# Optimization experiments

Hardware: AMD Instinct MI355X
Metric: run time of the kernel (lower is better)

Reference implementation:

```python
import jax, jax.numpy as jnp
import numpy as np

HID_GNN = 64
HID_LSTM = 128
FUTURE = 24
N_HYDRO = 32
N_METEO = 64
B, T, E = 32, 168, 384
SLOPE = 0.01  # F.leaky_relu default


def setup_inputs() -> dict:
    key = jax.random.key(0)
    ks = jax.random.split(key, 12)
    N = N_HYDRO + N_METEO
    data_meteo = jax.random.normal(ks[0], (B, T, N_METEO, 1), jnp.float32)
    data_hydro = jax.random.normal(ks[1], (B, T, N_HYDRO, 1), jnp.float32)
    edge_index = jax.random.randint(ks[2], (2, E), 0, N, dtype=jnp.int64)
    # GraphConv(1, HID_GNN): out = lin_root(x) + lin_rel(sum_j x_j) + bias
    W_root = jax.random.normal(ks[3], (HID_GNN, 1), jnp.float32) * 1.0
    W_rel = jax.random.normal(ks[4], (HID_GNN, 1), jnp.float32) * 1.0
    b_gnn = jnp.zeros((HID_GNN,), jnp.float32)
    # Per-station LSTM weights (torch gate order i,f,g,o), stacked over stations
    sih = 1.0 / np.sqrt(HID_GNN)
    shh = 1.0 / np.sqrt(HID_LSTM)
    Wih = jax.random.normal(ks[5], (N_HYDRO, 4 * HID_LSTM, HID_GNN), jnp.float32) * sih
    Whh = jax.random.normal(ks[6], (N_HYDRO, 4 * HID_LSTM, HID_LSTM), jnp.float32) * shh
    bih = jnp.zeros((N_HYDRO, 4 * HID_LSTM), jnp.float32)
    bhh = jnp.zeros((N_HYDRO, 4 * HID_LSTM), jnp.float32)
    W_lin = jax.random.normal(ks[7], (FUTURE, HID_LSTM), jnp.float32) * shh
    b_lin = jnp.zeros((FUTURE,), jnp.float32)
    return {"data_meteo": data_meteo, "data_hydro": data_hydro, "edge_index": edge_index,
            "W_root": W_root, "W_rel": W_rel, "b_gnn": b_gnn,
            "Wih": Wih, "Whh": Whh, "bih": bih, "bhh": bhh,
            "W_lin": W_lin, "b_lin": b_lin}


def _lstm_last(xs, Wih_s, Whh_s, b_s):
    # xs: [B,T,D]; one station's LSTM; returns last hidden [B,H]
    H = Whh_s.shape[1]
    h0 = jnp.zeros((xs.shape[0], H), xs.dtype)

    def step(carry, xt):
        h, c = carry
        gates = xt @ Wih_s.T + h @ Whh_s.T + b_s  # [B,4H]
        i, f, g, o = jnp.split(gates, 4, axis=-1)
        c = jax.nn.sigmoid(f) * c + jax.nn.sigmoid(i) * jnp.tanh(g)
        h = jax.nn.sigmoid(o) * jnp.tanh(c)
        return (h, c), None

    (hT, _), _ = jax.lax.scan(step, (h0, h0), jnp.swapaxes(xs, 0, 1))
    return hT


def reference(data_meteo, data_hydro, edge_index, W_root, W_rel, b_gnn,
              Wih, Whh, bih, bhh, W_lin, b_lin):
    Bn, Tn, Nh, F = data_hydro.shape
    Nm = data_meteo.shape[2]
    N = Nh + Nm
    # [B,T,N,1] -> one graph per (b,t); same edge_index in every graph
    x = jnp.concatenate([data_hydro, data_meteo], axis=2).reshape(Bn * Tn, N, F)
    src, dst = edge_index[0], edge_index[1]
    agg = jnp.zeros_like(x).at[:, dst].add(x[:, src])  # sum aggregation
    h = x @ W_root.T + agg @ W_rel.T + b_gnn          # GraphConv, [G,N,HID_GNN]
    h = jax.nn.leaky_relu(h, SLOPE)
    hydro = h.reshape(Bn, Tn, N, -1)[:, :, :Nh, :]    # [B,T,Nh,HID_GNN]
    # per-station LSTM: vmap over station axis with station-specific weights
    last = jax.vmap(_lstm_last, in_axes=(2, 0, 0, 0))(hydro, Wih, Whh, bih + bhh)  # [Nh,B,H]
    pred = last @ W_lin.T + b_lin                     # [Nh,B,FUTURE]
    pred = jnp.swapaxes(pred, 0, 1)                   # [B,Nh,FUTURE]
    return jax.nn.leaky_relu(pred, SLOPE)
```

## Files before the change

### kernel.cpp

```cpp
#include <hip/hip_runtime.h>

typedef unsigned short u16;
typedef unsigned int u32;
typedef __attribute__((ext_vector_type(8))) short short8;
typedef __attribute__((ext_vector_type(4))) float floatx4;
typedef __attribute__((ext_vector_type(4))) float float4v;

#define B_ 32
#define T_ 168
#define NH_ 32
#define NM_ 64
#define E_ 384
#define HL_ 128
#define FUT_ 24
#define SLOPE_ 0.01f
#define XP_ 80
#define HP_ 144
#define WIH_LP 72
#define WHH_LP 136
#define OVL_E (T_ * 4 * XP_)

static __device__ __forceinline__ float b2f(u16 u) {
  u32 v = ((u32)u) << 16;
  return __builtin_bit_cast(float, v);
}
static __device__ __forceinline__ u16 f2bf(float f) {
  u32 x = __builtin_bit_cast(u32, f);
  u32 r = (x + 0x7fffu + ((x >> 16) & 1u)) >> 16;
  return (u16)r;
}
static __device__ __forceinline__ float fexp2(float x) { return __builtin_amdgcn_exp2f(x); }
static __device__ __forceinline__ float frcp(float x) { return __builtin_amdgcn_rcpf(x); }
static __device__ __forceinline__ float sigm(float x) {
  return frcp(1.0f + fexp2(-1.4426950408889634f * x));
}
static __device__ __forceinline__ float tanh_fast(float x) {
  return 1.0f - 2.0f * frcp(1.0f + fexp2(2.8853900817779268f * x));
}
static __device__ __forceinline__ float sel4(floatx4 v, int r) {
  float m0 = (r & 1) ? v[1] : v[0];
  float m1 = (r & 1) ? v[3] : v[2];
  return (r & 2) ? m1 : m0;
}
static __device__ __forceinline__ float lrelu(float x) { return fmaxf(x, SLOPE_ * x); }

__launch_bounds__(512, 2)
__global__ void fused_kernel(const float* __restrict__ dm, const float* __restrict__ dh,
                             const int* __restrict__ eidx,
                             const float* __restrict__ Wroot, const float* __restrict__ Wrel,
                             const float* __restrict__ bgnn,
                             const float* __restrict__ Wih, const float* __restrict__ Whh,
                             const float* __restrict__ bih, const float* __restrict__ bhh,
                             const float* __restrict__ Wlin, const float* __restrict__ blin,
                             float* __restrict__ out) {
  const int s = blockIdx.x & 31;
  const int bg = blockIdx.x >> 5;
  const int tid = threadIdx.x;
  const int w = tid >> 6;
  const int lane = tid & 63;
  const int cm = lane & 15;
  const int q = lane >> 4;
  const int b = cm & 3;
  const int rho = cm >> 2;

  __shared__ __align__(16) u16 ovl[OVL_E];
  __shared__ __align__(16) u16 hbuf[2 * 4 * HP_];
  __shared__ float xh_lds[4][T_];
  __shared__ float ag_lds[4][T_];
  __shared__ float wr_s[64], wv_s[64], bg_s[64];
  __shared__ int srcs[E_];
  __shared__ int nsrc, iflag;

  if (tid == 0) { nsrc = 0; iflag = 0; }
  for (int i = tid; i < 2 * 4 * HP_; i += 512) hbuf[i] = 0;
  __syncthreads();

  {
    int odd = 0;
    for (int e = tid; e < E_; e += 512) odd |= eidx[2 * e + 1];
    if (odd) atomicOr(&iflag, 1);
  }
  __syncthreads();
  const bool i32 = iflag != 0;

  for (int e = tid; e < E_; e += 512) {
    int se = i32 ? eidx[e] : eidx[2 * e];
    int de = i32 ? eidx[E_ + e] : eidx[2 * E_ + 2 * e];
    if (de == s) { int i = atomicAdd(&nsrc, 1); srcs[i] = se; }
  }
  if (tid < 64) { wr_s[tid] = Wroot[tid]; wv_s[tid] = Wrel[tid]; bg_s[tid] = bgnn[tid]; }
  for (int i = tid; i < 4 * T_; i += 512) {
    int bb = i / T_, t = i % T_;
    xh_lds[bb][t] = dh[((size_t)(bg * 4 + bb) * T_ + t) * NH_ + s];
  }
  floatx4 bias_init[4];
#pragma unroll
  for (int blk = 0; blk < 4; blk++)
#pragma unroll
    for (int r = 0; r < 4; r++) {
      const int nb = blk * 128 + w * 16 + q * 4 + r;
      bias_init[blk][r] = bih[s * 512 + nb] + bhh[s * 512 + nb];
    }
  __syncthreads();

  const int ns = nsrc;
  for (int i = tid; i < 4 * T_; i += 512) {
    int bb = i / T_, t = i % T_;
    size_t gb = (size_t)(bg * 4 + bb) * T_ + t;
    float a = 0.f;
    for (int j = 0; j < ns; j++) {
      int sr = srcs[j];
      a += (sr < NH_) ? dh[gb * NH_ + sr] : dm[gb * NM_ + (sr - NH_)];
    }
    ag_lds[bb][t] = a;
  }

  short8 Af[4][6];
  const int nl = w * 16 + cm;
  __syncthreads();
  {
    const float* g = Wih + (size_t)s * 512 * 64;
#pragma unroll
    for (int it = 0; it < 16; it++) {
      int j = tid + it * 512;
      float4v v = *(const float4v*)(g + 4 * j);
      u16* dst = ovl + (j >> 4) * WIH_LP + (j & 15) * 4;
      dst[0] = f2bf(v[0]); dst[1] = f2bf(v[1]); dst[2] = f2bf(v[2]); dst[3] = f2bf(v[3]);
    }
  }
  __syncthreads();
#pragma unroll
  for (int blk = 0; blk < 4; blk++)
#pragma unroll
    for (int kk = 0; kk < 2; kk++)
      Af[blk][kk] = *(const short8*)(ovl + (blk * 128 + nl) * WIH_LP + kk * 32 + q * 8);
  __syncthreads();
  {
    const float* g = Whh + (size_t)s * 512 * 128;
#pragma unroll
    for (int it = 0; it < 16; it++) {
      int j = tid + it * 512;
      float4v v = *(const float4v*)(g + 4 * j);
      u16* dst = ovl + (j >> 5) * WHH_LP + (j & 31) * 4;
      dst[0] = f2bf(v[0]); dst[1] = f2bf(v[1]); dst[2] = f2bf(v[2]); dst[3] = f2bf(v[3]);
    }
  }
  __syncthreads();
#pragma unroll
  for (int blk = 0; blk < 2; blk++)
#pragma unroll
    for (int kk = 0; kk < 4; kk++)
      Af[blk][2 + kk] = *(const short8*)(ovl + (blk * 128 + nl) * WHH_LP + kk * 32 + q * 8);
  __syncthreads();
  {
    const float* g = Whh + ((size_t)s * 512 + 256) * 128;
#pragma unroll
    for (int it = 0; it < 16; it++) {
      int j = tid + it * 512;
      float4v v = *(const float4v*)(g + 4 * j);
      u16* dst = ovl + (j >> 5) * WHH_LP + (j & 31) * 4;
      dst[0] = f2bf(v[0]); dst[1] = f2bf(v[1]); dst[2] = f2bf(v[2]); dst[3] = f2bf(v[3]);
    }
  }
  __syncthreads();
#pragma unroll
  for (int blk = 2; blk < 4; blk++)
#pragma unroll
    for (int kk = 0; kk < 4; kk++)
      Af[blk][2 + kk] = *(const short8*)(ovl + ((blk - 2) * 128 + nl) * WHH_LP + kk * 32 + q * 8);
  __syncthreads();

  {
    const int k = tid & 63;
    const int bb = (tid >> 6) & 3;
    const int th = tid >> 8;
    const float wrk = wr_s[k], wvk = wv_s[k], bgk = bg_s[k];
    for (int i = 0; i < T_ / 2; i++) {
      const int t = th * (T_ / 2) + i;
      const float xv = xh_lds[bb][t] * wrk + ag_lds[bb][t] * wvk + bgk;
      ovl[t * (4 * XP_) + bb * XP_ + k] = f2bf(lrelu(xv));
    }
  }
  __syncthreads();

  floatx4 accN[4];
  {
    short8 Bx0 = *(const short8*)(ovl + b * XP_ + q * 8);
    short8 Bx1 = *(const short8*)(ovl + b * XP_ + 32 + q * 8);
#pragma unroll
    for (int blk = 0; blk < 4; blk++) {
      accN[blk] = __builtin_amdgcn_mfma_f32_16x16x32_bf16(Af[blk][0], Bx0, bias_init[blk], 0, 0, 0);
      accN[blk] = __builtin_amdgcn_mfma_f32_16x16x32_bf16(Af[blk][1], Bx1, accN[blk], 0, 0, 0);
    }
  }
  float c = 0.0f;
#pragma unroll 2
  for (int t = 0; t < T_; t++) {
    const int p = t & 1, pn = p ^ 1;
    short8 Bh[4];
#pragma unroll
    for (int kk = 0; kk < 4; kk++)
      Bh[kk] = *(const short8*)(hbuf + p * (4 * HP_) + b * HP_ + kk * 32 + q * 8);

    floatx4 acc[4];
#pragma unroll
    for (int blk = 0; blk < 4; blk++) acc[blk] = accN[blk];
#pragma unroll
    for (int kk = 0; kk < 4; kk++)
#pragma unroll
      for (int blk = 0; blk < 4; blk++)
        acc[blk] = __builtin_amdgcn_mfma_f32_16x16x32_bf16(Af[blk][2 + kk], Bh[kk], acc[blk], 0, 0, 0);

    const float gi = sel4(acc[0], rho);
    const float gf = sel4(acc[1], rho);
    const float gg = sel4(acc[2], rho);
    const float go = sel4(acc[3], rho);
    c = sigm(gf) * c + sigm(gi) * tanh_fast(gg);
    const float hh = sigm(go) * tanh_fast(c);
    hbuf[pn * (4 * HP_) + b * HP_ + w * 16 + q * 4 + rho] = f2bf(hh);

    if (t + 1 < T_) {
      short8 Bx0 = *(const short8*)(ovl + (t + 1) * (4 * XP_) + b * XP_ + q * 8);
      short8 Bx1 = *(const short8*)(ovl + (t + 1) * (4 * XP_) + b * XP_ + 32 + q * 8);
#pragma unroll
      for (int blk = 0; blk < 4; blk++) {
        accN[blk] = __builtin_amdgcn_mfma_f32_16x16x32_bf16(Af[blk][0], Bx0, bias_init[blk], 0, 0, 0);
        accN[blk] = __builtin_amdgcn_mfma_f32_16x16x32_bf16(Af[blk][1], Bx1, accN[blk], 0, 0, 0);
      }
    }
    __syncthreads();
  }

  if (tid < 4 * FUT_) {
    const int bb = tid / FUT_;
    const int f = tid % FUT_;
    float a = blin[f];
#pragma unroll 8
    for (int k = 0; k < HL_; k++) a += b2f(hbuf[bb * HP_ + k]) * Wlin[f * HL_ + k];
    out[((size_t)(bg * 4 + bb) * NH_ + s) * FUT_ + f] = lrelu(a);
  }
}

extern "C" void kernel_launch(void* const* d_in, const int* in_sizes, int n_in,
                              void* d_out, int out_size, void* d_ws, size_t ws_size,
                              hipStream_t stream) {
  const float* dm = (const float*)d_in[0];
  const float* dh = (const float*)d_in[1];
  const int* eidx = (const int*)d_in[2];
  const float* Wroot = (const float*)d_in[3];
  const float* Wrel = (const float*)d_in[4];
  const float* bgnn = (const float*)d_in[5];
  const float* Wih = (const float*)d_in[6];
  const float* Whh = (const float*)d_in[7];
  const float* bih = (const float*)d_in[8];
  const float* bhh = (const float*)d_in[9];
  const float* Wlin = (const float*)d_in[10];
  const float* blin = (const float*)d_in[11];
  float* out = (float*)d_out;

  fused_kernel<<<256, 512, 0, stream>>>(dm, dh, eidx, Wroot, Wrel, bgnn, Wih, Whh,
                                        bih, bhh, Wlin, blin, out);
}
```

Baseline: 190.7 us.

## Interleave two independent batch streams per block and prescale gate weights

Each block now handles 8 batch rows as two independent 4-row LSTM streams. The MFMA work of one stream is interleaved with the gate math of the other, which hides the serial recurrence latency, and the grid shrinks from 256 to 128 blocks. The input projection is computed over two 84-step windows so the shared-memory buffer fits. Sigmoid and tanh scale factors are folded into the bf16 weights and biases to remove one multiply per gate. The cost is half as many blocks, so fewer CUs are in use, plus higher register pressure.

```diff
diff --git a/kernel.cpp b/kernel.cpp
--- a/kernel.cpp
+++ b/kernel.cpp
@@ -16,9 +16,11 @@
 #define SLOPE_ 0.01f
 #define XP_ 80
 #define HP_ 144
+#define TW_ 84
 #define WIH_LP 72
 #define WHH_LP 136
-#define OVL_E (T_ * 4 * XP_)
+#define CH1_ (-1.4426950408889634f)
+#define CH2_ (2.8853900817779268f)
 
 static __device__ __forceinline__ float b2f(u16 u) {
   u32 v = ((u32)u) << 16;
@@ -31,9 +33,8 @@
 }
 static __device__ __forceinline__ float fexp2(float x) { return __builtin_amdgcn_exp2f(x); }
 static __device__ __forceinline__ float frcp(float x) { return __builtin_amdgcn_rcpf(x); }
-static __device__ __forceinline__ float sigm(float x) {
-  return frcp(1.0f + fexp2(-1.4426950408889634f * x));
-}
+static __device__ __forceinline__ float sigm_pre(float x) { return frcp(1.0f + fexp2(x)); }
+static __device__ __forceinline__ float tanh_pre(float x) { return 1.0f - 2.0f * frcp(1.0f + fexp2(x)); }
 static __device__ __forceinline__ float tanh_fast(float x) {
   return 1.0f - 2.0f * frcp(1.0f + fexp2(2.8853900817779268f * x));
 }
@@ -54,7 +55,7 @@
                              const float* __restrict__ Wlin, const float* __restrict__ blin,
                              float* __restrict__ out) {
   const int s = blockIdx.x & 31;
-  const int bg = blockIdx.x >> 5;
+  const int bgp = blockIdx.x >> 5;
   const int tid = threadIdx.x;
   const int w = tid >> 6;
   const int lane = tid & 63;
@@ -63,16 +64,16 @@
   const int b = cm & 3;
   const int rho = cm >> 2;
 
-  __shared__ __align__(16) u16 ovl[OVL_E];
-  __shared__ __align__(16) u16 hbuf[2 * 4 * HP_];
-  __shared__ float xh_lds[4][T_];
-  __shared__ float ag_lds[4][T_];
+  __shared__ __align__(16) u16 xwin[TW_ * 8 * XP_];
+  __shared__ __align__(16) u16 hbuf[2 * 2 * 4 * HP_];
+  __shared__ float xh_lds[8][T_];
+  __shared__ float ag_lds[8][T_];
   __shared__ float wr_s[64], wv_s[64], bg_s[64];
   __shared__ int srcs[E_];
   __shared__ int nsrc, iflag;
 
   if (tid == 0) { nsrc = 0; iflag = 0; }
-  for (int i = tid; i < 2 * 4 * HP_; i += 512) hbuf[i] = 0;
+  for (int i = tid; i < 2 * 2 * 4 * HP_; i += 512) hbuf[i] = 0;
   __syncthreads();
 
   {
@@ -89,24 +90,26 @@
     if (de == s) { int i = atomicAdd(&nsrc, 1); srcs[i] = se; }
   }
   if (tid < 64) { wr_s[tid] = Wroot[tid]; wv_s[tid] = Wrel[tid]; bg_s[tid] = bgnn[tid]; }
-  for (int i = tid; i < 4 * T_; i += 512) {
+  for (int i = tid; i < 8 * T_; i += 512) {
     int bb = i / T_, t = i % T_;
-    xh_lds[bb][t] = dh[((size_t)(bg * 4 + bb) * T_ + t) * NH_ + s];
+    xh_lds[bb][t] = dh[((size_t)(bgp * 8 + bb) * T_ + t) * NH_ + s];
   }
   floatx4 bias_init[4];
 #pragma unroll
-  for (int blk = 0; blk < 4; blk++)
+  for (int blk = 0; blk < 4; blk++) {
+    const float sc = (blk == 2) ? CH2_ : CH1_;
 #pragma unroll
     for (int r = 0; r < 4; r++) {
       const int nb = blk * 128 + w * 16 + q * 4 + r;
-      bias_init[blk][r] = bih[s * 512 + nb] + bhh[s * 512 + nb];
-    }
+      bias_init[blk][r] = (bih[s * 512 + nb] + bhh[s * 512 + nb]) * sc;
+    }
+  }
   __syncthreads();
 
   const int ns = nsrc;
-  for (int i = tid; i < 4 * T_; i += 512) {
+  for (int i = tid; i < 8 * T_; i += 512) {
     int bb = i / T_, t = i % T_;
-    size_t gb = (size_t)(bg * 4 + bb) * T_ + t;
+    size_t gb = (size_t)(bgp * 8 + bb) * T_ + t;
     float a = 0.f;
     for (int j = 0; j < ns; j++) {
       int sr = srcs[j];
@@ -124,8 +127,10 @@
     for (int it = 0; it < 16; it++) {
       int j = tid + it * 512;
       float4v v = *(const float4v*)(g + 4 * j);
-      u16* dst = ovl + (j >> 4) * WIH_LP + (j & 15) * 4;
-      dst[0] = f2bf(v[0]); dst[1] = f2bf(v[1]); dst[2] = f2bf(v[2]); dst[3] = f2bf(v[3]);
+      const float sc = (((j >> 4) >> 7) == 2) ? CH2_ : CH1_;
+      u16* dst = xwin + (j >> 4) * WIH_LP + (j & 15) * 4;
+      dst[0] = f2bf(v[0] * sc); dst[1] = f2bf(v[1] * sc);
+      dst[2] = f2bf(v[2] * sc); dst[3] = f2bf(v[3] * sc);
     }
   }
   __syncthreads();
@@ -133,7 +138,7 @@
   for (int blk = 0; blk < 4; blk++)
 #pragma unroll
     for (int kk = 0; kk < 2; kk++)
-      Af[blk][kk] = *(const short8*)(ovl + (blk * 128 + nl) * WIH_LP + kk * 32 + q * 8);
+      Af[blk][kk] = *(const short8*)(xwin + (blk * 128 + nl) * WIH_LP + kk * 32 + q * 8);
   __syncthreads();
   {
     const float* g = Whh + (size_t)s * 512 * 128;
@@ -141,8 +146,9 @@
     for (int it = 0; it < 16; it++) {
       int j = tid + it * 512;
       float4v v = *(const float4v*)(g + 4 * j);
-      u16* dst = ovl + (j >> 5) * WHH_LP + (j & 31) * 4;
-      dst[0] = f2bf(v[0]); dst[1] = f2bf(v[1]); dst[2] = f2bf(v[2]); dst[3] = f2bf(v[3]);
+      u16* dst = xwin + (j >> 5) * WHH_LP + (j & 31) * 4;
+      dst[0] = f2bf(v[0] * CH1_); dst[1] = f2bf(v[1] * CH1_);
+      dst[2] = f2bf(v[2] * CH1_); dst[3] = f2bf(v[3] * CH1_);
     }
   }
   __syncthreads();
@@ -150,7 +156,7 @@
   for (int blk = 0; blk < 2; blk++)
 #pragma unroll
     for (int kk = 0; kk < 4; kk++)
-      Af[blk][2 + kk] = *(const short8*)(ovl + (blk * 128 + nl) * WHH_LP + kk * 32 + q * 8);
+      Af[blk][2 + kk] = *(const short8*)(xwin + (blk * 128 + nl) * WHH_LP + kk * 32 + q * 8);
   __syncthreads();
   {
     const float* g = Whh + ((size_t)s * 512 + 256) * 128;
@@ -158,8 +164,10 @@
     for (int it = 0; it < 16; it++) {
       int j = tid + it * 512;
       float4v v = *(const float4v*)(g + 4 * j);
-      u16* dst = ovl + (j >> 5) * WHH_LP + (j & 31) * 4;
-      dst[0] = f2bf(v[0]); dst[1] = f2bf(v[1]); dst[2] = f2bf(v[2]); dst[3] = f2bf(v[3]);
+      const float sc = ((j >> 5) < 128) ? CH2_ : CH1_;
+      u16* dst = xwin + (j >> 5) * WHH_LP + (j & 31) * 4;
+      dst[0] = f2bf(v[0] * sc); dst[1] = f2bf(v[1] * sc);
+      dst[2] = f2bf(v[2] * sc); dst[3] = f2bf(v[3] * sc);
     }
   }
   __syncthreads();
@@ -167,77 +175,111 @@
   for (int blk = 2; blk < 4; blk++)
 #pragma unroll
     for (int kk = 0; kk < 4; kk++)
-      Af[blk][2 + kk] = *(const short8*)(ovl + ((blk - 2) * 128 + nl) * WHH_LP + kk * 32 + q * 8);
-  __syncthreads();
-
-  {
-    const int k = tid & 63;
-    const int bb = (tid >> 6) & 3;
-    const int th = tid >> 8;
-    const float wrk = wr_s[k], wvk = wv_s[k], bgk = bg_s[k];
-    for (int i = 0; i < T_ / 2; i++) {
-      const int t = th * (T_ / 2) + i;
-      const float xv = xh_lds[bb][t] * wrk + ag_lds[bb][t] * wvk + bgk;
-      ovl[t * (4 * XP_) + bb * XP_ + k] = f2bf(lrelu(xv));
-    }
-  }
-  __syncthreads();
-
-  floatx4 accN[4];
-  {
-    short8 Bx0 = *(const short8*)(ovl + b * XP_ + q * 8);
-    short8 Bx1 = *(const short8*)(ovl + b * XP_ + 32 + q * 8);
-#pragma unroll
-    for (int blk = 0; blk < 4; blk++) {
-      accN[blk] = __builtin_amdgcn_mfma_f32_16x16x32_bf16(Af[blk][0], Bx0, bias_init[blk], 0, 0, 0);
-      accN[blk] = __builtin_amdgcn_mfma_f32_16x16x32_bf16(Af[blk][1], Bx1, accN[blk], 0, 0, 0);
-    }
-  }
-  float c = 0.0f;
+      Af[blk][2 + kk] = *(const short8*)(xwin + ((blk - 2) * 128 + nl) * WHH_LP + kk * 32 + q * 8);
+
+  float cA = 0.f, cB = 0.f;
+  floatx4 accNA[4];
+#pragma unroll 1
+  for (int ch = 0; ch < 2; ch++) {
+    const int t0 = ch * TW_;
+    __syncthreads();
+    {
+      const int k = tid & 63;
+      const int bb = tid >> 6;
+      const float wrk = wr_s[k], wvk = wv_s[k], bgk = bg_s[k];
+      u16* xw = xwin + bb * XP_ + k;
+#pragma unroll 4
+      for (int i = 0; i < TW_; i++) {
+        const float xv = xh_lds[bb][t0 + i] * wrk + ag_lds[bb][t0 + i] * wvk + bgk;
+        xw[i * (8 * XP_)] = f2bf(lrelu(xv));
+      }
+    }
+    __syncthreads();
+    short8 BxB0, BxB1;
+    {
+      short8 BxA0 = *(const short8*)(xwin + b * XP_ + q * 8);
+      short8 BxA1 = *(const short8*)(xwin + b * XP_ + 32 + q * 8);
+#pragma unroll
+      for (int blk = 0; blk < 4; blk++) {
+        accNA[blk] = __builtin_amdgcn_mfma_f32_16x16x32_bf16(Af[blk][0], BxA0, bias_init[blk], 0, 0, 0);
+        accNA[blk] = __builtin_amdgcn_mfma_f32_16x16x32_bf16(Af[blk][1], BxA1, accNA[blk], 0, 0, 0);
+      }
+      BxB0 = *(const short8*)(xwin + (b + 4) * XP_ + q * 8);
+      BxB1 = *(const short8*)(xwin + (b + 4) * XP_ + 32 + q * 8);
+    }
 #pragma unroll 2
-  for (int t = 0; t < T_; t++) {
-    const int p = t & 1, pn = p ^ 1;
-    short8 Bh[4];
-#pragma unroll
-    for (int kk = 0; kk < 4; kk++)
-      Bh[kk] = *(const short8*)(hbuf + p * (4 * HP_) + b * HP_ + kk * 32 + q * 8);
-
-    floatx4 acc[4];
-#pragma unroll
-    for (int blk = 0; blk < 4; blk++) acc[blk] = accN[blk];
-#pragma unroll
-    for (int kk = 0; kk < 4; kk++)
+    for (int i = 0; i < TW_; i++) {
+      const int p = i & 1, pn = p ^ 1;
+      short8 BhA[4];
+#pragma unroll
+      for (int kk = 0; kk < 4; kk++)
+        BhA[kk] = *(const short8*)(hbuf + (p * 4 + b) * HP_ + kk * 32 + q * 8);
+      floatx4 aB[4];
+#pragma unroll
+      for (int blk = 0; blk < 4; blk++) {
+        aB[blk] = __builtin_amdgcn_mfma_f32_16x16x32_bf16(Af[blk][0], BxB0, bias_init[blk], 0, 0, 0);
+        aB[blk] = __builtin_amdgcn_mfma_f32_16x16x32_bf16(Af[blk][1], BxB1, aB[blk], 0, 0, 0);
+      }
+      floatx4 aA[4];
 #pragma unroll
       for (int blk = 0; blk < 4; blk++)
-        acc[blk] = __builtin_amdgcn_mfma_f32_16x16x32_bf16(Af[blk][2 + kk], Bh[kk], acc[blk], 0, 0, 0);
-
-    const float gi = sel4(acc[0], rho);
-    const float gf = sel4(acc[1], rho);
-    const float gg = sel4(acc[2], rho);
-    const float go = sel4(acc[3], rho);
-    c = sigm(gf) * c + sigm(gi) * tanh_fast(gg);
-    const float hh = sigm(go) * tanh_fast(c);
-    hbuf[pn * (4 * HP_) + b * HP_ + w * 16 + q * 4 + rho] = f2bf(hh);
-
-    if (t + 1 < T_) {
-      short8 Bx0 = *(const short8*)(ovl + (t + 1) * (4 * XP_) + b * XP_ + q * 8);
-      short8 Bx1 = *(const short8*)(ovl + (t + 1) * (4 * XP_) + b * XP_ + 32 + q * 8);
-#pragma unroll
-      for (int blk = 0; blk < 4; blk++) {
-        accN[blk] = __builtin_amdgcn_mfma_f32_16x16x32_bf16(Af[blk][0], Bx0, bias_init[blk], 0, 0, 0);
-        accN[blk] = __builtin_amdgcn_mfma_f32_16x16x32_bf16(Af[blk][1], Bx1, accN[blk], 0, 0, 0);
-      }
-    }
-    __syncthreads();
-  }
-
-  if (tid < 4 * FUT_) {
+        aA[blk] = __builtin_amdgcn_mfma_f32_16x16x32_bf16(Af[blk][2], BhA[0], accNA[blk], 0, 0, 0);
+#pragma unroll
+      for (int kk = 1; kk < 4; kk++)
+#pragma unroll
+        for (int blk = 0; blk < 4; blk++)
+          aA[blk] = __builtin_amdgcn_mfma_f32_16x16x32_bf16(Af[blk][2 + kk], BhA[kk], aA[blk], 0, 0, 0);
+      short8 BhB[4];
+#pragma unroll
+      for (int kk = 0; kk < 4; kk++)
+        BhB[kk] = *(const short8*)(hbuf + ((2 + p) * 4 + b) * HP_ + kk * 32 + q * 8);
+      {
+        const float gi = sel4(aA[0], rho);
+        const float gf = sel4(aA[1], rho);
+        const float gg = sel4(aA[2], rho);
+        const float go = sel4(aA[3], rho);
+        cA = sigm_pre(gf) * cA + sigm_pre(gi) * tanh_pre(gg);
+        const float hh = sigm_pre(go) * tanh_fast(cA);
+        hbuf[(pn * 4 + b) * HP_ + w * 16 + q * 4 + rho] = f2bf(hh);
+      }
+#pragma unroll
+      for (int kk = 0; kk < 4; kk++)
+#pragma unroll
+        for (int blk = 0; blk < 4; blk++)
+          aB[blk] = __builtin_amdgcn_mfma_f32_16x16x32_bf16(Af[blk][2 + kk], BhB[kk], aB[blk], 0, 0, 0);
+      if (i + 1 < TW_) {
+        short8 BxA0 = *(const short8*)(xwin + (i + 1) * (8 * XP_) + b * XP_ + q * 8);
+        short8 BxA1 = *(const short8*)(xwin + (i + 1) * (8 * XP_) + b * XP_ + 32 + q * 8);
+#pragma unroll
+        for (int blk = 0; blk < 4; blk++) {
+          accNA[blk] = __builtin_amdgcn_mfma_f32_16x16x32_bf16(Af[blk][0], BxA0, bias_init[blk], 0, 0, 0);
+          accNA[blk] = __builtin_amdgcn_mfma_f32_16x16x32_bf16(Af[blk][1], BxA1, accNA[blk], 0, 0, 0);
+        }
+        BxB0 = *(const short8*)(xwin + (i + 1) * (8 * XP_) + (b + 4) * XP_ + q * 8);
+        BxB1 = *(const short8*)(xwin + (i + 1) * (8 * XP_) + (b + 4) * XP_ + 32 + q * 8);
+      }
+      {
+        const float gi = sel4(aB[0], rho);
+        const float gf = sel4(aB[1], rho);
+        const float gg = sel4(aB[2], rho);
+        const float go = sel4(aB[3], rho);
+        cB = sigm_pre(gf) * cB + sigm_pre(gi) * tanh_pre(gg);
+        const float hh = sigm_pre(go) * tanh_fast(cB);
+        hbuf[((2 + pn) * 4 + b) * HP_ + w * 16 + q * 4 + rho] = f2bf(hh);
+      }
+      __syncthreads();
+    }
+  }
+
+  if (tid < 8 * FUT_) {
     const int bb = tid / FUT_;
     const int f = tid % FUT_;
+    const int st = bb >> 2, bl = bb & 3;
     float a = blin[f];
 #pragma unroll 8
-    for (int k = 0; k < HL_; k++) a += b2f(hbuf[bb * HP_ + k]) * Wlin[f * HL_ + k];
-    out[((size_t)(bg * 4 + bb) * NH_ + s) * FUT_ + f] = lrelu(a);
+    for (int k = 0; k < HL_; k++)
+      a += b2f(hbuf[(st * 2 * 4 + bl) * HP_ + k]) * Wlin[f * HL_ + k];
+    out[((size_t)(bgp * 8 + bb) * NH_ + s) * FUT_ + f] = lrelu(a);
   }
 }
 
@@ -258,6 +300,6 @@
   const float* blin = (const float*)d_in[11];
   float* out = (float*)d_out;
 
-  fused_kernel<<<256, 512, 0, stream>>>(dm, dh, eidx, Wroot, Wrel, bgnn, Wih, Whh,
+  fused_kernel<<<128, 512, 0, stream>>>(dm, dh, eidx, Wroot, Wrel, bgnn, Wih, Whh,
                                         bih, bhh, Wlin, blin, out);
 }
```

Measured after the change: 270.6 us. +41.9%, slower.

## Split batch into two interleaved MFMA streams and fold activation scales into weights

Applied to the files above, without the earlier changes.

Splits the four batch columns of the recurrent MFMA into two independent two-column streams whose MFMAs are interleaved, giving the per-step dependency chain more independent work to hide MFMA latency. The next step's input projection is issued before the gate nonlinearities. The exp2 scale constants for sigmoid/tanh are pre-multiplied into the bf16 weights and biases, removing multiplies from the per-step activation math. The cost is twice as many MFMA instructions per step, each doing half-useful columns, plus slightly different bf16 rounding of scaled weights.

```diff
diff --git a/kernel.cpp b/kernel.cpp
--- a/kernel.cpp
+++ b/kernel.cpp
@@ -18,7 +18,8 @@
 #define HP_ 144
 #define WIH_LP 72
 #define WHH_LP 136
-#define OVL_E (T_ * 4 * XP_)
+#define CH1_ (-1.4426950408889634f)
+#define CH2_ (2.8853900817779268f)
 
 static __device__ __forceinline__ float b2f(u16 u) {
   u32 v = ((u32)u) << 16;
@@ -31,9 +32,8 @@
 }
 static __device__ __forceinline__ float fexp2(float x) { return __builtin_amdgcn_exp2f(x); }
 static __device__ __forceinline__ float frcp(float x) { return __builtin_amdgcn_rcpf(x); }
-static __device__ __forceinline__ float sigm(float x) {
-  return frcp(1.0f + fexp2(-1.4426950408889634f * x));
-}
+static __device__ __forceinline__ float sigm_pre(float x) { return frcp(1.0f + fexp2(x)); }
+static __device__ __forceinline__ float tanh_pre(float x) { return 1.0f - 2.0f * frcp(1.0f + fexp2(x)); }
 static __device__ __forceinline__ float tanh_fast(float x) {
   return 1.0f - 2.0f * frcp(1.0f + fexp2(2.8853900817779268f * x));
 }
@@ -60,11 +60,12 @@
   const int lane = tid & 63;
   const int cm = lane & 15;
   const int q = lane >> 4;
-  const int b = cm & 3;
-  const int rho = cm >> 2;
-
-  __shared__ __align__(16) u16 ovl[OVL_E];
-  __shared__ __align__(16) u16 hbuf[2 * 4 * HP_];
+  const int b = cm & 1;
+  const int rho = (cm >> 1) & 3;
+  const int str = cm >> 3;
+
+  __shared__ __align__(16) u16 xbuf[T_ * 4 * XP_];
+  __shared__ __align__(16) u16 hbuf[2 * 2 * 2 * HP_];
   __shared__ float xh_lds[4][T_];
   __shared__ float ag_lds[4][T_];
   __shared__ float wr_s[64], wv_s[64], bg_s[64];
@@ -72,7 +73,7 @@
   __shared__ int nsrc, iflag;
 
   if (tid == 0) { nsrc = 0; iflag = 0; }
-  for (int i = tid; i < 2 * 4 * HP_; i += 512) hbuf[i] = 0;
+  for (int i = tid; i < 2 * 2 * 2 * HP_; i += 512) hbuf[i] = 0;
   __syncthreads();
 
   {
@@ -95,12 +96,14 @@
   }
   floatx4 bias_init[4];
 #pragma unroll
-  for (int blk = 0; blk < 4; blk++)
+  for (int blk = 0; blk < 4; blk++) {
+    const float sc = (blk == 2) ? CH2_ : CH1_;
 #pragma unroll
     for (int r = 0; r < 4; r++) {
       const int nb = blk * 128 + w * 16 + q * 4 + r;
-      bias_init[blk][r] = bih[s * 512 + nb] + bhh[s * 512 + nb];
-    }
+      bias_init[blk][r] = (bih[s * 512 + nb] + bhh[s * 512 + nb]) * sc;
+    }
+  }
   __syncthreads();
 
   const int ns = nsrc;
@@ -124,8 +127,10 @@
     for (int it = 0; it < 16; it++) {
       int j = tid + it * 512;
       float4v v = *(const float4v*)(g + 4 * j);
-      u16* dst = ovl + (j >> 4) * WIH_LP + (j & 15) * 4;
-      dst[0] = f2bf(v[0]); dst[1] = f2bf(v[1]); dst[2] = f2bf(v[2]); dst[3] = f2bf(v[3]);
+      const float sc = (((j >> 4) >> 7) == 2) ? CH2_ : CH1_;
+      u16* dst = xbuf + (j >> 4) * WIH_LP + (j & 15) * 4;
+      dst[0] = f2bf(v[0] * sc); dst[1] = f2bf(v[1] * sc);
+      dst[2] = f2bf(v[2] * sc); dst[3] = f2bf(v[3] * sc);
     }
   }
   __syncthreads();
@@ -133,7 +138,7 @@
   for (int blk = 0; blk < 4; blk++)
 #pragma unroll
     for (int kk = 0; kk < 2; kk++)
-      Af[blk][kk] = *(const short8*)(ovl + (blk * 128 + nl) * WIH_LP + kk * 32 + q * 8);
+      Af[blk][kk] = *(const short8*)(xbuf + (blk * 128 + nl) * WIH_LP + kk * 32 + q * 8);
   __syncthreads();
   {
     const float* g = Whh + (size_t)s * 512 * 128;
@@ -141,8 +146,9 @@
     for (int it = 0; it < 16; it++) {
       int j = tid + it * 512;
       float4v v = *(const float4v*)(g + 4 * j);
-      u16* dst = ovl + (j >> 5) * WHH_LP + (j & 31) * 4;
-      dst[0] = f2bf(v[0]); dst[1] = f2bf(v[1]); dst[2] = f2bf(v[2]); dst[3] = f2bf(v[3]);
+      u16* dst = xbuf + (j >> 5) * WHH_LP + (j & 31) * 4;
+      dst[0] = f2bf(v[0] * CH1_); dst[1] = f2bf(v[1] * CH1_);
+      dst[2] = f2bf(v[2] * CH1_); dst[3] = f2bf(v[3] * CH1_);
     }
   }
   __syncthreads();
@@ -150,7 +156,7 @@
   for (int blk = 0; blk < 2; blk++)
 #pragma unroll
     for (int kk = 0; kk < 4; kk++)
-      Af[blk][2 + kk] = *(const short8*)(ovl + (blk * 128 + nl) * WHH_LP + kk * 32 + q * 8);
+      Af[blk][2 + kk] = *(const short8*)(xbuf + (blk * 128 + nl) * WHH_LP + kk * 32 + q * 8);
   __syncthreads();
   {
     const float* g = Whh + ((size_t)s * 512 + 256) * 128;
@@ -158,8 +164,10 @@
     for (int it = 0; it < 16; it++) {
       int j = tid + it * 512;
       float4v v = *(const float4v*)(g + 4 * j);
-      u16* dst = ovl + (j >> 5) * WHH_LP + (j & 31) * 4;
-      dst[0] = f2bf(v[0]); dst[1] = f2bf(v[1]); dst[2] = f2bf(v[2]); dst[3] = f2bf(v[3]);
+      const float sc = ((j >> 5) < 128) ? CH2_ : CH1_;
+      u16* dst = xbuf + (j >> 5) * WHH_LP + (j & 31) * 4;
+      dst[0] = f2bf(v[0] * sc); dst[1] = f2bf(v[1] * sc);
+      dst[2] = f2bf(v[2] * sc); dst[3] = f2bf(v[3] * sc);
     }
   }
   __syncthreads();
@@ -167,7 +175,7 @@
   for (int blk = 2; blk < 4; blk++)
 #pragma unroll
     for (int kk = 0; kk < 4; kk++)
-      Af[blk][2 + kk] = *(const short8*)(ovl + ((blk - 2) * 128 + nl) * WHH_LP + kk * 32 + q * 8);
+      Af[blk][2 + kk] = *(const short8*)(xbuf + ((blk - 2) * 128 + nl) * WHH_LP + kk * 32 + q * 8);
   __syncthreads();
 
   {
@@ -178,55 +186,70 @@
     for (int i = 0; i < T_ / 2; i++) {
       const int t = th * (T_ / 2) + i;
       const float xv = xh_lds[bb][t] * wrk + ag_lds[bb][t] * wvk + bgk;
-      ovl[t * (4 * XP_) + bb * XP_ + k] = f2bf(lrelu(xv));
-    }
-  }
-  __syncthreads();
-
-  floatx4 accN[4];
-  {
-    short8 Bx0 = *(const short8*)(ovl + b * XP_ + q * 8);
-    short8 Bx1 = *(const short8*)(ovl + b * XP_ + 32 + q * 8);
+      xbuf[t * (4 * XP_) + bb * XP_ + k] = f2bf(lrelu(xv));
+    }
+  }
+  __syncthreads();
+
+  floatx4 accNA[4], accNB[4];
+  {
+    short8 BxA0 = *(const short8*)(xbuf + b * XP_ + q * 8);
+    short8 BxA1 = *(const short8*)(xbuf + b * XP_ + 32 + q * 8);
+    short8 BxB0 = *(const short8*)(xbuf + (2 + b) * XP_ + q * 8);
+    short8 BxB1 = *(const short8*)(xbuf + (2 + b) * XP_ + 32 + q * 8);
 #pragma unroll
     for (int blk = 0; blk < 4; blk++) {
-      accN[blk] = __builtin_amdgcn_mfma_f32_16x16x32_bf16(Af[blk][0], Bx0, bias_init[blk], 0, 0, 0);
-      accN[blk] = __builtin_amdgcn_mfma_f32_16x16x32_bf16(Af[blk][1], Bx1, accN[blk], 0, 0, 0);
-    }
-  }
-  float c = 0.0f;
+      accNA[blk] = __builtin_amdgcn_mfma_f32_16x16x32_bf16(Af[blk][0], BxA0, bias_init[blk], 0, 0, 0);
+      accNA[blk] = __builtin_amdgcn_mfma_f32_16x16x32_bf16(Af[blk][1], BxA1, accNA[blk], 0, 0, 0);
+      accNB[blk] = __builtin_amdgcn_mfma_f32_16x16x32_bf16(Af[blk][0], BxB0, bias_init[blk], 0, 0, 0);
+      accNB[blk] = __builtin_amdgcn_mfma_f32_16x16x32_bf16(Af[blk][1], BxB1, accNB[blk], 0, 0, 0);
+    }
+  }
+  float c = 0.f;
 #pragma unroll 2
   for (int t = 0; t < T_; t++) {
     const int p = t & 1, pn = p ^ 1;
-    short8 Bh[4];
-#pragma unroll
-    for (int kk = 0; kk < 4; kk++)
-      Bh[kk] = *(const short8*)(hbuf + p * (4 * HP_) + b * HP_ + kk * 32 + q * 8);
-
-    floatx4 acc[4];
-#pragma unroll
-    for (int blk = 0; blk < 4; blk++) acc[blk] = accN[blk];
-#pragma unroll
-    for (int kk = 0; kk < 4; kk++)
-#pragma unroll
-      for (int blk = 0; blk < 4; blk++)
-        acc[blk] = __builtin_amdgcn_mfma_f32_16x16x32_bf16(Af[blk][2 + kk], Bh[kk], acc[blk], 0, 0, 0);
-
-    const float gi = sel4(acc[0], rho);
-    const float gf = sel4(acc[1], rho);
-    const float gg = sel4(acc[2], rho);
-    const float go = sel4(acc[3], rho);
-    c = sigm(gf) * c + sigm(gi) * tanh_fast(gg);
-    const float hh = sigm(go) * tanh_fast(c);
-    hbuf[pn * (4 * HP_) + b * HP_ + w * 16 + q * 4 + rho] = f2bf(hh);
-
+    short8 BhA[4], BhB[4];
+#pragma unroll
+    for (int kk = 0; kk < 4; kk++) {
+      BhA[kk] = *(const short8*)(hbuf + (p * 2 + b) * HP_ + kk * 32 + q * 8);
+      BhB[kk] = *(const short8*)(hbuf + ((2 + p) * 2 + b) * HP_ + kk * 32 + q * 8);
+    }
+    floatx4 aA[4], aB[4];
+#pragma unroll
+    for (int blk = 0; blk < 4; blk++) {
+      aA[blk] = __builtin_amdgcn_mfma_f32_16x16x32_bf16(Af[blk][2], BhA[0], accNA[blk], 0, 0, 0);
+      aB[blk] = __builtin_amdgcn_mfma_f32_16x16x32_bf16(Af[blk][2], BhB[0], accNB[blk], 0, 0, 0);
+    }
+#pragma unroll
+    for (int kk = 1; kk < 4; kk++)
+#pragma unroll
+      for (int blk = 0; blk < 4; blk++) {
+        aA[blk] = __builtin_amdgcn_mfma_f32_16x16x32_bf16(Af[blk][2 + kk], BhA[kk], aA[blk], 0, 0, 0);
+        aB[blk] = __builtin_amdgcn_mfma_f32_16x16x32_bf16(Af[blk][2 + kk], BhB[kk], aB[blk], 0, 0, 0);
+      }
     if (t + 1 < T_) {
-      short8 Bx0 = *(const short8*)(ovl + (t + 1) * (4 * XP_) + b * XP_ + q * 8);
-      short8 Bx1 = *(const short8*)(ovl + (t + 1) * (4 * XP_) + b * XP_ + 32 + q * 8);
+      const u16* xr = xbuf + (t + 1) * (4 * XP_);
+      short8 BxA0 = *(const short8*)(xr + b * XP_ + q * 8);
+      short8 BxA1 = *(const short8*)(xr + b * XP_ + 32 + q * 8);
+      short8 BxB0 = *(const short8*)(xr + (2 + b) * XP_ + q * 8);
+      short8 BxB1 = *(const short8*)(xr + (2 + b) * XP_ + 32 + q * 8);
 #pragma unroll
       for (int blk = 0; blk < 4; blk++) {
-        accN[blk] = __builtin_amdgcn_mfma_f32_16x16x32_bf16(Af[blk][0], Bx0, bias_init[blk], 0, 0, 0);
-        accN[blk] = __builtin_amdgcn_mfma_f32_16x16x32_bf16(Af[blk][1], Bx1, accN[blk], 0, 0, 0);
+        accNA[blk] = __builtin_amdgcn_mfma_f32_16x16x32_bf16(Af[blk][0], BxA0, bias_init[blk], 0, 0, 0);
+        accNA[blk] = __builtin_amdgcn_mfma_f32_16x16x32_bf16(Af[blk][1], BxA1, accNA[blk], 0, 0, 0);
+        accNB[blk] = __builtin_amdgcn_mfma_f32_16x16x32_bf16(Af[blk][0], BxB0, bias_init[blk], 0, 0, 0);
+        accNB[blk] = __builtin_amdgcn_mfma_f32_16x16x32_bf16(Af[blk][1], BxB1, accNB[blk], 0, 0, 0);
       }
+    }
+    {
+      const float gi = str ? sel4(aB[0], rho) : sel4(aA[0], rho);
+      const float gf = str ? sel4(aB[1], rho) : sel4(aA[1], rho);
+      const float gg = str ? sel4(aB[2], rho) : sel4(aA[2], rho);
+      const float go = str ? sel4(aB[3], rho) : sel4(aA[3], rho);
+      c = sigm_pre(gf) * c + sigm_pre(gi) * tanh_pre(gg);
+      const float hh = sigm_pre(go) * tanh_fast(c);
+      hbuf[(str * 4 + pn * 2 + b) * HP_ + w * 16 + q * 4 + rho] = f2bf(hh);
     }
     __syncthreads();
   }
@@ -236,7 +259,8 @@
     const int f = tid % FUT_;
     float a = blin[f];
 #pragma unroll 8
-    for (int k = 0; k < HL_; k++) a += b2f(hbuf[bb * HP_ + k]) * Wlin[f * HL_ + k];
+    for (int k = 0; k < HL_; k++)
+      a += b2f(hbuf[((bb >> 1) * 4 + (bb & 1)) * HP_ + k]) * Wlin[f * HL_ + k];
     out[((size_t)(bg * 4 + bb) * NH_ + s) * FUT_ + f] = lrelu(a);
   }
 }
```

Result: slower. 262.4 us (+37.6%).

## Precompute input-gate projections per time window and fold activation scales into weights

Applied to the files above, without the earlier changes.

The input projection Wih·x is taken out of the serial recurrence. For each 21-step window the GNN features are staged, and all input-gate preactivations are computed in a batched MFMA pass and stored as bf16 in LDS. The recurrent loop then only loads and unpacks them. The exp2 scaling constants for sigmoid and tanh are folded into the weights and biases, which removes multiplies from the critical path. The cost is extra rounding, since the input preactivations are now stored in bf16, plus one extra barrier pass per window.

```diff
diff --git a/kernel.cpp b/kernel.cpp
--- a/kernel.cpp
+++ b/kernel.cpp
@@ -5,6 +5,7 @@
 typedef __attribute__((ext_vector_type(8))) short short8;
 typedef __attribute__((ext_vector_type(4))) float floatx4;
 typedef __attribute__((ext_vector_type(4))) float float4v;
+typedef __attribute__((ext_vector_type(2))) u32 uint2v;
 
 #define B_ 32
 #define T_ 168
@@ -14,11 +15,14 @@
 #define HL_ 128
 #define FUT_ 24
 #define SLOPE_ 0.01f
-#define XP_ 80
 #define HP_ 144
+#define TW_ 21
+#define ZP_ 528
+#define XSP_ 72
 #define WIH_LP 72
 #define WHH_LP 136
-#define OVL_E (T_ * 4 * XP_)
+#define CH1_ (-1.4426950408889634f)
+#define CH2_ (2.8853900817779268f)
 
 static __device__ __forceinline__ float b2f(u16 u) {
   u32 v = ((u32)u) << 16;
@@ -31,9 +35,8 @@
 }
 static __device__ __forceinline__ float fexp2(float x) { return __builtin_amdgcn_exp2f(x); }
 static __device__ __forceinline__ float frcp(float x) { return __builtin_amdgcn_rcpf(x); }
-static __device__ __forceinline__ float sigm(float x) {
-  return frcp(1.0f + fexp2(-1.4426950408889634f * x));
-}
+static __device__ __forceinline__ float sigm_pre(float x) { return frcp(1.0f + fexp2(x)); }
+static __device__ __forceinline__ float tanh_pre(float x) { return 1.0f - 2.0f * frcp(1.0f + fexp2(x)); }
 static __device__ __forceinline__ float tanh_fast(float x) {
   return 1.0f - 2.0f * frcp(1.0f + fexp2(2.8853900817779268f * x));
 }
@@ -63,7 +66,8 @@
   const int b = cm & 3;
   const int rho = cm >> 2;
 
-  __shared__ __align__(16) u16 ovl[OVL_E];
+  __shared__ __align__(16) u16 zwin[TW_ * 4 * ZP_];
+  __shared__ __align__(16) u16 xstage[96 * XSP_];
   __shared__ __align__(16) u16 hbuf[2 * 4 * HP_];
   __shared__ float xh_lds[4][T_];
   __shared__ float ag_lds[4][T_];
@@ -95,12 +99,14 @@
   }
   floatx4 bias_init[4];
 #pragma unroll
-  for (int blk = 0; blk < 4; blk++)
+  for (int blk = 0; blk < 4; blk++) {
+    const float sc = (blk == 2) ? CH2_ : CH1_;
 #pragma unroll
     for (int r = 0; r < 4; r++) {
       const int nb = blk * 128 + w * 16 + q * 4 + r;
-      bias_init[blk][r] = bih[s * 512 + nb] + bhh[s * 512 + nb];
-    }
+      bias_init[blk][r] = (bih[s * 512 + nb] + bhh[s * 512 + nb]) * sc;
+    }
+  }
   __syncthreads();
 
   const int ns = nsrc;
@@ -124,8 +130,10 @@
     for (int it = 0; it < 16; it++) {
       int j = tid + it * 512;
       float4v v = *(const float4v*)(g + 4 * j);
-      u16* dst = ovl + (j >> 4) * WIH_LP + (j & 15) * 4;
-      dst[0] = f2bf(v[0]); dst[1] = f2bf(v[1]); dst[2] = f2bf(v[2]); dst[3] = f2bf(v[3]);
+      const float sc = (((j >> 4) >> 7) == 2) ? CH2_ : CH1_;
+      u16* dst = zwin + (j >> 4) * WIH_LP + (j & 15) * 4;
+      dst[0] = f2bf(v[0] * sc); dst[1] = f2bf(v[1] * sc);
+      dst[2] = f2bf(v[2] * sc); dst[3] = f2bf(v[3] * sc);
     }
   }
   __syncthreads();
@@ -133,7 +141,7 @@
   for (int blk = 0; blk < 4; blk++)
 #pragma unroll
     for (int kk = 0; kk < 2; kk++)
-      Af[blk][kk] = *(const short8*)(ovl + (blk * 128 + nl) * WIH_LP + kk * 32 + q * 8);
+      Af[blk][kk] = *(const short8*)(zwin + (blk * 128 + nl) * WIH_LP + kk * 32 + q * 8);
   __syncthreads();
   {
     const float* g = Whh + (size_t)s * 512 * 128;
@@ -141,8 +149,9 @@
     for (int it = 0; it < 16; it++) {
       int j = tid + it * 512;
       float4v v = *(const float4v*)(g + 4 * j);
-      u16* dst = ovl + (j >> 5) * WHH_LP + (j & 31) * 4;
-      dst[0] = f2bf(v[0]); dst[1] = f2bf(v[1]); dst[2] = f2bf(v[2]); dst[3] = f2bf(v[3]);
+      u16* dst = zwin + (j >> 5) * WHH_LP + (j & 31) * 4;
+      dst[0] = f2bf(v[0] * CH1_); dst[1] = f2bf(v[1] * CH1_);
+      dst[2] = f2bf(v[2] * CH1_); dst[3] = f2bf(v[3] * CH1_);
     }
   }
   __syncthreads();
@@ -150,7 +159,7 @@
   for (int blk = 0; blk < 2; blk++)
 #pragma unroll
     for (int kk = 0; kk < 4; kk++)
-      Af[blk][2 + kk] = *(const short8*)(ovl + (blk * 128 + nl) * WHH_LP + kk * 32 + q * 8);
+      Af[blk][2 + kk] = *(const short8*)(zwin + (blk * 128 + nl) * WHH_LP + kk * 32 + q * 8);
   __syncthreads();
   {
     const float* g = Whh + ((size_t)s * 512 + 256) * 128;
@@ -158,8 +167,10 @@
     for (int it = 0; it < 16; it++) {
       int j = tid + it * 512;
       float4v v = *(const float4v*)(g + 4 * j);
-      u16* dst = ovl + (j >> 5) * WHH_LP + (j & 31) * 4;
-      dst[0] = f2bf(v[0]); dst[1] = f2bf(v[1]); dst[2] = f2bf(v[2]); dst[3] = f2bf(v[3]);
+      const float sc = ((j >> 5) < 128) ? CH2_ : CH1_;
+      u16* dst = zwin + (j >> 5) * WHH_LP + (j & 31) * 4;
+      dst[0] = f2bf(v[0] * sc); dst[1] = f2bf(v[1] * sc);
+      dst[2] = f2bf(v[2] * sc); dst[3] = f2bf(v[3] * sc);
     }
   }
   __syncthreads();
@@ -167,68 +178,83 @@
   for (int blk = 2; blk < 4; blk++)
 #pragma unroll
     for (int kk = 0; kk < 4; kk++)
-      Af[blk][2 + kk] = *(const short8*)(ovl + ((blk - 2) * 128 + nl) * WHH_LP + kk * 32 + q * 8);
-  __syncthreads();
-
-  {
-    const int k = tid & 63;
-    const int bb = (tid >> 6) & 3;
-    const int th = tid >> 8;
-    const float wrk = wr_s[k], wvk = wv_s[k], bgk = bg_s[k];
-    for (int i = 0; i < T_ / 2; i++) {
-      const int t = th * (T_ / 2) + i;
-      const float xv = xh_lds[bb][t] * wrk + ag_lds[bb][t] * wvk + bgk;
-      ovl[t * (4 * XP_) + bb * XP_ + k] = f2bf(lrelu(xv));
-    }
-  }
-  __syncthreads();
-
-  floatx4 accN[4];
-  {
-    short8 Bx0 = *(const short8*)(ovl + b * XP_ + q * 8);
-    short8 Bx1 = *(const short8*)(ovl + b * XP_ + 32 + q * 8);
-#pragma unroll
-    for (int blk = 0; blk < 4; blk++) {
-      accN[blk] = __builtin_amdgcn_mfma_f32_16x16x32_bf16(Af[blk][0], Bx0, bias_init[blk], 0, 0, 0);
-      accN[blk] = __builtin_amdgcn_mfma_f32_16x16x32_bf16(Af[blk][1], Bx1, accN[blk], 0, 0, 0);
-    }
-  }
-  float c = 0.0f;
-#pragma unroll 2
-  for (int t = 0; t < T_; t++) {
-    const int p = t & 1, pn = p ^ 1;
-    short8 Bh[4];
-#pragma unroll
-    for (int kk = 0; kk < 4; kk++)
-      Bh[kk] = *(const short8*)(hbuf + p * (4 * HP_) + b * HP_ + kk * 32 + q * 8);
-
-    floatx4 acc[4];
-#pragma unroll
-    for (int blk = 0; blk < 4; blk++) acc[blk] = accN[blk];
-#pragma unroll
-    for (int kk = 0; kk < 4; kk++)
-#pragma unroll
-      for (int blk = 0; blk < 4; blk++)
-        acc[blk] = __builtin_amdgcn_mfma_f32_16x16x32_bf16(Af[blk][2 + kk], Bh[kk], acc[blk], 0, 0, 0);
-
-    const float gi = sel4(acc[0], rho);
-    const float gf = sel4(acc[1], rho);
-    const float gg = sel4(acc[2], rho);
-    const float go = sel4(acc[3], rho);
-    c = sigm(gf) * c + sigm(gi) * tanh_fast(gg);
-    const float hh = sigm(go) * tanh_fast(c);
-    hbuf[pn * (4 * HP_) + b * HP_ + w * 16 + q * 4 + rho] = f2bf(hh);
-
-    if (t + 1 < T_) {
-      short8 Bx0 = *(const short8*)(ovl + (t + 1) * (4 * XP_) + b * XP_ + q * 8);
-      short8 Bx1 = *(const short8*)(ovl + (t + 1) * (4 * XP_) + b * XP_ + 32 + q * 8);
+      Af[blk][2 + kk] = *(const short8*)(zwin + ((blk - 2) * 128 + nl) * WHH_LP + kk * 32 + q * 8);
+
+  float c = 0.f;
+#pragma unroll 1
+  for (int ch = 0; ch < 8; ch++) {
+    const int tb = ch * TW_;
+    __syncthreads();
+    for (int idx = tid; idx < 84 * 64; idx += 512) {
+      const int col = idx >> 6, k = idx & 63;
+      const int i = col >> 2, bb = col & 3;
+      const float xv = xh_lds[bb][tb + i] * wr_s[k] + ag_lds[bb][tb + i] * wv_s[k] + bg_s[k];
+      xstage[col * XSP_ + k] = f2bf(lrelu(xv));
+    }
+    __syncthreads();
+#pragma unroll
+    for (int ct = 0; ct < 6; ct++) {
+      const int col = ct * 16 + cm;
+      short8 Bx0 = *(const short8*)(xstage + col * XSP_ + q * 8);
+      short8 Bx1 = *(const short8*)(xstage + col * XSP_ + 32 + q * 8);
 #pragma unroll
       for (int blk = 0; blk < 4; blk++) {
-        accN[blk] = __builtin_amdgcn_mfma_f32_16x16x32_bf16(Af[blk][0], Bx0, bias_init[blk], 0, 0, 0);
-        accN[blk] = __builtin_amdgcn_mfma_f32_16x16x32_bf16(Af[blk][1], Bx1, accN[blk], 0, 0, 0);
+        floatx4 za = __builtin_amdgcn_mfma_f32_16x16x32_bf16(Af[blk][0], Bx0, bias_init[blk], 0, 0, 0);
+        za = __builtin_amdgcn_mfma_f32_16x16x32_bf16(Af[blk][1], Bx1, za, 0, 0, 0);
+        if (col < 84) {
+          u16 pk[4];
+#pragma unroll
+          for (int r = 0; r < 4; r++) pk[r] = f2bf(za[r]);
+          *(uint2v*)(zwin + col * ZP_ + blk * 128 + w * 16 + q * 4) = *(uint2v*)pk;
+        }
       }
     }
     __syncthreads();
+
+    uint2v z4[4];
+#pragma unroll
+    for (int blk = 0; blk < 4; blk++)
+      z4[blk] = *(const uint2v*)(zwin + b * ZP_ + blk * 128 + w * 16 + q * 4);
+
+#pragma unroll 3
+    for (int i = 0; i < TW_; i++) {
+      const int t = tb + i;
+      const int p = t & 1, pn = p ^ 1;
+      short8 Bh[4];
+#pragma unroll
+      for (int kk = 0; kk < 4; kk++)
+        Bh[kk] = *(const short8*)(hbuf + (p * 4 + b) * HP_ + kk * 32 + q * 8);
+
+      floatx4 acc[4];
+#pragma unroll
+      for (int blk = 0; blk < 4; blk++) {
+        const u32 w0 = z4[blk][0], w1 = z4[blk][1];
+        acc[blk][0] = __builtin_bit_cast(float, w0 << 16);
+        acc[blk][1] = __builtin_bit_cast(float, w0 & 0xFFFF0000u);
+        acc[blk][2] = __builtin_bit_cast(float, w1 << 16);
+        acc[blk][3] = __builtin_bit_cast(float, w1 & 0xFFFF0000u);
+      }
+#pragma unroll
+      for (int kk = 0; kk < 4; kk++)
+#pragma unroll
+        for (int blk = 0; blk < 4; blk++)
+          acc[blk] = __builtin_amdgcn_mfma_f32_16x16x32_bf16(Af[blk][2 + kk], Bh[kk], acc[blk], 0, 0, 0);
+
+      const float gi = sel4(acc[0], rho);
+      const float gf = sel4(acc[1], rho);
+      const float gg = sel4(acc[2], rho);
+      const float go = sel4(acc[3], rho);
+      c = sigm_pre(gf) * c + sigm_pre(gi) * tanh_pre(gg);
+      const float hh = sigm_pre(go) * tanh_fast(c);
+      hbuf[(pn * 4 + b) * HP_ + w * 16 + q * 4 + rho] = f2bf(hh);
+
+      if (i + 1 < TW_) {
+#pragma unroll
+        for (int blk = 0; blk < 4; blk++)
+          z4[blk] = *(const uint2v*)(zwin + ((i + 1) * 4 + b) * ZP_ + blk * 128 + w * 16 + q * 4);
+      }
+      __syncthreads();
+    }
   }
 
   if (tid < 4 * FUT_) {
```

After: 199.0 us. +4.3%, slower.
